# Performance work log

Hardware: AMD Instinct MI355X
Metric: run time of the kernel (lower is better)

The kernel has to match this reference:

```python
import jax, jax.numpy as jnp
import numpy as np

N_NODES = 50000
N_EDGES = 600000
IN_DIM = 128
FEAT = 128
N_CLS = 40


def _lin_params(key, fan_in, fan_out, bias=True):
    k1, k2 = jax.random.split(key)
    lim = 1.0 / np.sqrt(fan_in)
    W = jax.random.uniform(k1, (fan_out, fan_in), jnp.float32, -lim, lim)
    b = jax.random.uniform(k2, (fan_out,), jnp.float32, -lim, lim) if bias else None
    return W, b


def setup_inputs() -> dict:
    key = jax.random.key(0)
    ks = jax.random.split(key, 8)
    x = jax.random.normal(ks[0], (N_NODES, IN_DIM), jnp.float32)
    edge_index = jax.random.randint(ks[1], (2, N_EDGES), 0, N_NODES, jnp.int64 if jax.config.read('jax_enable_x64') else jnp.int32)
    Wl1, bl1 = _lin_params(ks[2], IN_DIM, FEAT)
    Wr1, _ = _lin_params(ks[3], IN_DIM, FEAT, bias=False)
    Wl2, bl2 = _lin_params(ks[4], FEAT, FEAT)
    Wr2, _ = _lin_params(ks[5], FEAT, FEAT, bias=False)
    Wl3, bl3 = _lin_params(ks[6], FEAT, FEAT)
    Wr3, _ = _lin_params(ks[7], FEAT, FEAT, bias=False)
    kc = jax.random.fold_in(key, 99)
    Wc, bc = _lin_params(kc, FEAT, N_CLS)
    return {"x": x, "edge_index": edge_index,
            "Wl1": Wl1, "bl1": bl1, "Wr1": Wr1,
            "Wl2": Wl2, "bl2": bl2, "Wr2": Wr2,
            "Wl3": Wl3, "bl3": bl3, "Wr3": Wr3,
            "Wc": Wc, "bc": bc}


def _sage_relu(x, src, dst, deg_inv, Wl, bl, Wr):
    # mean aggregation over incoming neighbors: gather at src, scatter-add at dst
    agg = jax.ops.segment_sum(x[src], dst, num_segments=N_NODES)  # [N, F]
    agg = agg * deg_inv[:, None]
    out = agg @ Wl.T + bl + x @ Wr.T  # W1*mean(neigh) + W2*x_root
    return jax.nn.relu(out)


def reference(x, edge_index, Wl1, bl1, Wr1, Wl2, bl2, Wr2, Wl3, bl3, Wr3, Wc, bc):
    src, dst = edge_index[0], edge_index[1]
    deg = jax.ops.segment_sum(jnp.ones((src.shape[0],), x.dtype), dst, num_segments=N_NODES)
    deg_inv = 1.0 / jnp.maximum(deg, 1.0)
    local_repr = _sage_relu(x, src, dst, deg_inv, Wl1, bl1, Wr1)
    global_repr = _sage_relu(local_repr, src, dst, deg_inv, Wl2, bl2, Wr2)
    # invariant_feature_extractor: one SAGEConvwithRelu + (eval-mode) dropout + residual
    h = _sage_relu(global_repr, src, dst, deg_inv, Wl3, bl3, Wr3)
    vanilla_if = h + global_repr
    vanilla_pred = vanilla_if @ Wc.T + bc
    return vanilla_pred
```

## Files before the change

### kernel.cpp

```cpp
#include <hip/hip_runtime.h>
#include <hip/hip_bf16.h>

constexpr int N_NODES = 50000;
constexpr int N_EDGES = 600000;
constexpr int D       = 128;
constexpr int N_CLS   = 40;

using bf16x8 = __attribute__((ext_vector_type(8))) short;
using f32x4  = __attribute__((ext_vector_type(4))) float;

__device__ inline unsigned short f2bf(float f) {
    __hip_bfloat16 h = __float2bfloat16(f);
    return __builtin_bit_cast(unsigned short, h);
}
__device__ inline float bf2f(unsigned short u) {
    __hip_bfloat16 h = __builtin_bit_cast(__hip_bfloat16, u);
    return __bfloat162float(h);
}


__global__ void hist_kernel(const int* __restrict__ ei, int* __restrict__ cnt) {
    int e = blockIdx.x * 256 + threadIdx.x;
    if (e < N_EDGES) atomicAdd(&cnt[ei[N_EDGES + e]], 1);
}

__global__ __launch_bounds__(1024) void scan_block_kernel(const int* __restrict__ cnt,
                                                          int* __restrict__ rs,
                                                          int* __restrict__ bsum, int n) {
    __shared__ int t[1024];
    int tid = threadIdx.x;
    int gid = blockIdx.x * 1024 + tid;
    int v = (gid < n) ? cnt[gid] : 0;
    t[tid] = v;
    __syncthreads();
    for (int off = 1; off < 1024; off <<= 1) {
        int u = (tid >= off) ? t[tid - off] : 0;
        __syncthreads();
        t[tid] += u;
        __syncthreads();
    }
    if (gid < n) rs[gid] = t[tid] - v;
    if (tid == 1023) bsum[blockIdx.x] = t[1023];
}

__global__ void scan_sums_kernel(const int* __restrict__ bsum, int* __restrict__ boff, int nblk) {
    __shared__ int t[64];
    int tid = threadIdx.x;
    int v = (tid < nblk) ? bsum[tid] : 0;
    t[tid] = v;
    __syncthreads();
    for (int off = 1; off < 64; off <<= 1) {
        int u = (tid >= off) ? t[tid - off] : 0;
        __syncthreads();
        t[tid] += u;
        __syncthreads();
    }
    if (tid < nblk) boff[tid] = t[tid] - v;
}

__global__ void finalize_kernel(const int* __restrict__ cnt, int* __restrict__ rs,
                                int* __restrict__ cursor, float* __restrict__ dinv,
                                const int* __restrict__ boff) {
    int i = blockIdx.x * 256 + threadIdx.x;
    if (i < N_NODES) {
        int v = rs[i] + boff[i >> 10];
        rs[i] = v;
        cursor[i] = v;
        dinv[i] = 1.0f / fmaxf((float)cnt[i], 1.0f);
        if (i == 0) rs[N_NODES] = N_EDGES;
    }
}

__global__ void scatter_kernel(const int* __restrict__ ei, int* __restrict__ cursor,
                               int* __restrict__ csr) {
    int e = blockIdx.x * 256 + threadIdx.x;
    if (e < N_EDGES) {
        int d = ei[N_EDGES + e];
        int p = atomicAdd(&cursor[d], 1);
        csr[p] = ei[e];
    }
}

__global__ void split_w_kernel(const float* __restrict__ Wl, const float* __restrict__ Wr,
                               unsigned short* __restrict__ hi, unsigned short* __restrict__ lo) {
    int idx = blockIdx.x * 256 + threadIdx.x;
    int n = idx >> 8, k = idx & 255;
    float v = (k < 128) ? Wl[n * 128 + k] : Wr[n * 128 + (k - 128)];
    unsigned short h = f2bf(v);
    hi[idx] = h;
    lo[idx] = f2bf(v - bf2f(h));
}

__global__ __launch_bounds__(256) void agg_kernel(const float* __restrict__ feat,
                                                  const int* __restrict__ rs,
                                                  const int* __restrict__ csr,
                                                  const float* __restrict__ dinv,
                                                  float* __restrict__ aggn) {
    int wave = threadIdx.x >> 6;
    int lane = threadIdx.x & 63;
    int node = blockIdx.x * 4 + wave;
    if (node >= N_NODES) return;
    int e0 = rs[node], e1 = rs[node + 1];
    float ax = 0.f, ay = 0.f;
    int e = e0;
    for (; e + 4 <= e1; e += 4) {
        int s0 = csr[e], s1 = csr[e + 1], s2 = csr[e + 2], s3 = csr[e + 3];
        float2 v0 = *(const float2*)&feat[(size_t)s0 * D + lane * 2];
        float2 v1 = *(const float2*)&feat[(size_t)s1 * D + lane * 2];
        float2 v2 = *(const float2*)&feat[(size_t)s2 * D + lane * 2];
        float2 v3 = *(const float2*)&feat[(size_t)s3 * D + lane * 2];
        ax += v0.x + v1.x + v2.x + v3.x;
        ay += v0.y + v1.y + v2.y + v3.y;
    }
    for (; e < e1; ++e) {
        int s = csr[e];
        float2 v = *(const float2*)&feat[(size_t)s * D + lane * 2];
        ax += v.x; ay += v.y;
    }
    float di = dinv[node];
    float2 o; o.x = ax * di; o.y = ay * di;
    *(float2*)&aggn[(size_t)node * D + lane * 2] = o;
}

__global__ __launch_bounds__(256) void gemm_mfma_kernel(const float* __restrict__ Aagg,
                                                        const float* __restrict__ Ax,
                                                        const unsigned short* __restrict__ Whi,
                                                        const unsigned short* __restrict__ Wlo,
                                                        const float* __restrict__ bias,
                                                        const float* __restrict__ resid,
                                                        float* __restrict__ outp, int M) {
    __shared__ __align__(16) unsigned short AhS[64 * 64];
    __shared__ __align__(16) unsigned short AlS[64 * 64];
    __shared__ __align__(16) unsigned short WhS[128 * 64];
    __shared__ __align__(16) unsigned short WlS[128 * 64];
    char* AhB = (char*)AhS;
    char* AlB = (char*)AlS;
    char* WhB = (char*)WhS;
    char* WlB = (char*)WlS;

    int tid = threadIdx.x;
    int lane = tid & 63;
    int wid = tid >> 6;
    int wr = wid >> 1;
    int wc = wid & 1;
    int lr = lane & 15;
    int kg = (lane >> 4) * 8;
    int row0 = blockIdx.x * 64;

    f32x4 acc[2][4];
#pragma unroll
    for (int f = 0; f < 2; ++f)
#pragma unroll
        for (int j = 0; j < 4; ++j) acc[f][j] = (f32x4){0.f, 0.f, 0.f, 0.f};

    for (int kt = 0; kt < 4; ++kt) {
        const float* Asrc = (kt < 2) ? Aagg : Ax;
        int kcol = (kt & 1) * 64;

#pragma unroll
        for (int it = 0; it < 2; ++it) {
            int slot = tid + it * 256;
            int row = slot >> 3;
            int k8 = (slot & 7) * 8;
            int gr = row0 + row;
            if (gr >= M) gr = M - 1;
            const float* p = &Asrc[(size_t)gr * D + kcol + k8];
            float4 v0 = *(const float4*)p;
            float4 v1 = *(const float4*)(p + 4);
            float fv[8] = {v0.x, v0.y, v0.z, v0.w, v1.x, v1.y, v1.z, v1.w};
            union { unsigned short u[8]; uint4 q; } ph, pl;
#pragma unroll
            for (int j = 0; j < 8; ++j) {
                unsigned short h = f2bf(fv[j]);
                ph.u[j] = h;
                pl.u[j] = f2bf(fv[j] - bf2f(h));
            }
            int boff = (row << 7) + (k8 << 1);
            boff ^= (row & 7) << 4;
            *(uint4*)(AhB + boff) = ph.q;
            *(uint4*)(AlB + boff) = pl.q;
        }
#pragma unroll
        for (int it = 0; it < 4; ++it) {
            int slot = tid + it * 256;
            int n = slot >> 3;
            int k8 = (slot & 7) * 8;
            size_t gsrc = (size_t)n * 256 + kt * 64 + k8;
            uint4 h = *(const uint4*)&Whi[gsrc];
            uint4 l = *(const uint4*)&Wlo[gsrc];
            int boff = (n << 7) + (k8 << 1);
            boff ^= (n & 7) << 4;
            *(uint4*)(WhB + boff) = h;
            *(uint4*)(WlB + boff) = l;
        }
        __syncthreads();

#pragma unroll
        for (int ks = 0; ks < 2; ++ks) {
            int kk = ks * 32 + kg;
            bf16x8 ah[2], al[2];
#pragma unroll
            for (int f = 0; f < 2; ++f) {
                int row = wr * 32 + f * 16 + lr;
                int boff = (row << 7) + (kk << 1);
                boff ^= (row & 7) << 4;
                ah[f] = *(const bf16x8*)(AhB + boff);
                al[f] = *(const bf16x8*)(AlB + boff);
            }
            bf16x8 bh[4], bl[4];
#pragma unroll
            for (int j = 0; j < 4; ++j) {
                int n = wc * 64 + j * 16 + lr;
                int boff = (n << 7) + (kk << 1);
                boff ^= (n & 7) << 4;
                bh[j] = *(const bf16x8*)(WhB + boff);
                bl[j] = *(const bf16x8*)(WlB + boff);
            }
#pragma unroll
            for (int f = 0; f < 2; ++f)
#pragma unroll
                for (int j = 0; j < 4; ++j) {
                    acc[f][j] = __builtin_amdgcn_mfma_f32_16x16x32_bf16(ah[f], bh[j], acc[f][j], 0, 0, 0);
                    acc[f][j] = __builtin_amdgcn_mfma_f32_16x16x32_bf16(ah[f], bl[j], acc[f][j], 0, 0, 0);
                    acc[f][j] = __builtin_amdgcn_mfma_f32_16x16x32_bf16(al[f], bh[j], acc[f][j], 0, 0, 0);
                }
        }
        __syncthreads();
    }

#pragma unroll
    for (int f = 0; f < 2; ++f)
#pragma unroll
        for (int j = 0; j < 4; ++j) {
            int c = wc * 64 + j * 16 + lr;
            float b = bias[c];
#pragma unroll
            for (int r = 0; r < 4; ++r) {
                int gr = row0 + wr * 32 + f * 16 + (lane >> 4) * 4 + r;
                if (gr < M) {
                    float v = acc[f][j][r] + b;
                    v = fmaxf(v, 0.f);
                    if (resid) v += resid[(size_t)gr * D + c];
                    outp[(size_t)gr * D + c] = v;
                }
            }
        }
}

__global__ __launch_bounds__(256) void classifier_kernel(const float* __restrict__ vif,
                                                         const float* __restrict__ Wc,
                                                         const float* __restrict__ bc,
                                                         float* __restrict__ outp, int M) {
    __shared__ float Vs[64][D + 4];
    __shared__ float Cs[N_CLS][D + 4];
    int tid = threadIdx.x;
    int row0 = blockIdx.x * 64;

#pragma unroll
    for (int l = 0; l < 8; ++l) {
        int slot = tid + l * 256;
        int r = slot >> 5;
        int kq = slot & 31;
        int gr = row0 + r;
        if (gr >= M) gr = M - 1;
        float4 v = *(const float4*)&vif[(size_t)gr * D + kq * 4];
        *(float4*)&Vs[r][kq * 4] = v;
    }
#pragma unroll
    for (int l = 0; l < 5; ++l) {
        int slot = tid + l * 256;
        int r = slot >> 5;
        int kq = slot & 31;
        float4 v = *(const float4*)&Wc[r * D + kq * 4];
        *(float4*)&Cs[r][kq * 4] = v;
    }
    __syncthreads();

    int r2 = tid >> 3;
    int cg = tid & 7;
    float acc[2][5] = {};
#pragma unroll 4
    for (int k4 = 0; k4 < 32; ++k4) {
        float4 a0 = *(const float4*)&Vs[r2 * 2][k4 * 4];
        float4 a1 = *(const float4*)&Vs[r2 * 2 + 1][k4 * 4];
#pragma unroll
        for (int j = 0; j < 5; ++j) {
            float4 w = *(const float4*)&Cs[cg * 5 + j][k4 * 4];
            acc[0][j] = fmaf(a0.x, w.x, fmaf(a0.y, w.y, fmaf(a0.z, w.z, fmaf(a0.w, w.w, acc[0][j]))));
            acc[1][j] = fmaf(a1.x, w.x, fmaf(a1.y, w.y, fmaf(a1.z, w.z, fmaf(a1.w, w.w, acc[1][j]))));
        }
    }
#pragma unroll
    for (int i = 0; i < 2; ++i) {
        int r = row0 + r2 * 2 + i;
        if (r >= M) continue;
#pragma unroll
        for (int j = 0; j < 5; ++j) {
            int c = cg * 5 + j;
            outp[(size_t)r * N_CLS + c] = acc[i][j] + bc[c];
        }
    }
}

extern "C" void kernel_launch(void* const* d_in, const int* in_sizes, int n_in,
                              void* d_out, int out_size, void* d_ws, size_t ws_size,
                              hipStream_t stream) {
    const float* x   = (const float*)d_in[0];
    const int*   ei  = (const int*)d_in[1];
    const float* Wl1 = (const float*)d_in[2];
    const float* bl1 = (const float*)d_in[3];
    const float* Wr1 = (const float*)d_in[4];
    const float* Wl2 = (const float*)d_in[5];
    const float* bl2 = (const float*)d_in[6];
    const float* Wr2 = (const float*)d_in[7];
    const float* Wl3 = (const float*)d_in[8];
    const float* bl3 = (const float*)d_in[9];
    const float* Wr3 = (const float*)d_in[10];
    const float* Wc  = (const float*)d_in[11];
    const float* bc  = (const float*)d_in[12];
    float* out = (float*)d_out;

    char* w = (char*)d_ws;
    size_t off = 0;
    auto carve = [&](size_t bytes) -> void* {
        void* p = w + off;
        off = (off + bytes + 255) & ~(size_t)255;
        return p;
    };
    int*   cnt    = (int*)carve((size_t)N_NODES * 4);
    int*   rs     = (int*)carve((size_t)(N_NODES + 1) * 4);
    int*   cursor = (int*)carve((size_t)N_NODES * 4);
    float* dinv   = (float*)carve((size_t)N_NODES * 4);
    int*   bsum   = (int*)carve(64 * 4);
    int*   boff   = (int*)carve(64 * 4);
    int*   csr    = (int*)carve((size_t)N_EDGES * 4);
    float* aggn   = (float*)carve((size_t)N_NODES * D * 4);
    float* bufA   = (float*)carve((size_t)N_NODES * D * 4);
    float* bufB   = (float*)carve((size_t)N_NODES * D * 4);
    unsigned short* w1h = (unsigned short*)carve(128 * 256 * 2);
    unsigned short* w1l = (unsigned short*)carve(128 * 256 * 2);
    unsigned short* w2h = (unsigned short*)carve(128 * 256 * 2);
    unsigned short* w2l = (unsigned short*)carve(128 * 256 * 2);
    unsigned short* w3h = (unsigned short*)carve(128 * 256 * 2);
    unsigned short* w3l = (unsigned short*)carve(128 * 256 * 2);
    (void)ws_size;

    const int NBLK_SCAN = (N_NODES + 1023) / 1024;
    const int GRID_E = (N_EDGES + 255) / 256;
    const int GRID_N = (N_NODES + 255) / 256;
    const int GRID_AGG = (N_NODES + 3) / 4;
    const int GRID_GEMM = (N_NODES + 63) / 64;

    hipMemsetAsync(cnt, 0, (size_t)N_NODES * 4, stream);
    hipLaunchKernelGGL(hist_kernel, dim3(GRID_E), dim3(256), 0, stream, ei, cnt);
    hipLaunchKernelGGL(split_w_kernel, dim3(128), dim3(256), 0, stream, Wl1, Wr1, w1h, w1l);
    hipLaunchKernelGGL(split_w_kernel, dim3(128), dim3(256), 0, stream, Wl2, Wr2, w2h, w2l);
    hipLaunchKernelGGL(split_w_kernel, dim3(128), dim3(256), 0, stream, Wl3, Wr3, w3h, w3l);
    hipLaunchKernelGGL(scan_block_kernel, dim3(NBLK_SCAN), dim3(1024), 0, stream, cnt, rs, bsum, N_NODES);
    hipLaunchKernelGGL(scan_sums_kernel, dim3(1), dim3(64), 0, stream, bsum, boff, NBLK_SCAN);
    hipLaunchKernelGGL(finalize_kernel, dim3(GRID_N), dim3(256), 0, stream, cnt, rs, cursor, dinv, boff);
    hipLaunchKernelGGL(scatter_kernel, dim3(GRID_E), dim3(256), 0, stream, ei, cursor, csr);

    hipLaunchKernelGGL(agg_kernel, dim3(GRID_AGG), dim3(256), 0, stream, x, rs, csr, dinv, aggn);
    hipLaunchKernelGGL(gemm_mfma_kernel, dim3(GRID_GEMM), dim3(256), 0, stream,
                       aggn, x, w1h, w1l, bl1, (const float*)nullptr, bufA, N_NODES);
    hipLaunchKernelGGL(agg_kernel, dim3(GRID_AGG), dim3(256), 0, stream, bufA, rs, csr, dinv, aggn);
    hipLaunchKernelGGL(gemm_mfma_kernel, dim3(GRID_GEMM), dim3(256), 0, stream,
                       aggn, bufA, w2h, w2l, bl2, (const float*)nullptr, bufB, N_NODES);
    hipLaunchKernelGGL(agg_kernel, dim3(GRID_AGG), dim3(256), 0, stream, bufB, rs, csr, dinv, aggn);
    hipLaunchKernelGGL(gemm_mfma_kernel, dim3(GRID_GEMM), dim3(256), 0, stream,
                       aggn, bufB, w3h, w3l, bl3, bufB, bufA, N_NODES);
    hipLaunchKernelGGL(classifier_kernel, dim3(GRID_GEMM), dim3(256), 0, stream,
                       bufA, Wc, bc, out, N_NODES);
}
```

Baseline: 391.0 us.

## Fuse neighbor aggregation into SAGE GEMM and fold classifier into last layer

Mean aggregation now runs inside the MFMA GEMM kernel: each block gathers neighbor rows via CSR into shared memory as split bf16 hi/lo tiles. This removes the aggn intermediate and its global write and read. The third layer also applies the residual and runs the classifier with MFMA in the same kernel, so bufA and the separate classifier launch are gone. Weight splitting is batched into fewer launches. In exchange, per-block gather work is serialized (16 nodes per wave), which may reduce memory-level parallelism compared with the separate agg kernel, and shared memory rises to 64KB per block, which limits occupancy.

```diff
diff --git a/kernel.cpp b/kernel.cpp
--- a/kernel.cpp
+++ b/kernel.cpp
@@ -81,62 +81,168 @@
     }
 }
 
-__global__ void split_w_kernel(const float* __restrict__ Wl, const float* __restrict__ Wr,
-                               unsigned short* __restrict__ hi, unsigned short* __restrict__ lo) {
+__global__ void split_w3_kernel(const float* __restrict__ Wl1, const float* __restrict__ Wr1,
+                                const float* __restrict__ Wl2, const float* __restrict__ Wr2,
+                                const float* __restrict__ Wl3, const float* __restrict__ Wr3,
+                                unsigned short* __restrict__ hi, unsigned short* __restrict__ lo) {
+    int layer = blockIdx.x >> 7;
+    int idx = (blockIdx.x & 127) * 256 + threadIdx.x;
+    int n = idx >> 8, k = idx & 255;
+    const float* Wl = (layer == 0) ? Wl1 : (layer == 1) ? Wl2 : Wl3;
+    const float* Wr = (layer == 0) ? Wr1 : (layer == 1) ? Wr2 : Wr3;
+    float v = (k < 128) ? Wl[n * 128 + k] : Wr[n * 128 + (k - 128)];
+    unsigned short h = f2bf(v);
+    size_t o = (size_t)layer * 32768 + idx;
+    hi[o] = h;
+    lo[o] = f2bf(v - bf2f(h));
+}
+
+__global__ void split_wc_kernel(const float* __restrict__ Wc,
+                                unsigned short* __restrict__ hi, unsigned short* __restrict__ lo) {
     int idx = blockIdx.x * 256 + threadIdx.x;
-    int n = idx >> 8, k = idx & 255;
-    float v = (k < 128) ? Wl[n * 128 + k] : Wr[n * 128 + (k - 128)];
+    int n = idx >> 7, k = idx & 127;
+    float v = (n < N_CLS) ? Wc[n * 128 + k] : 0.f;
     unsigned short h = f2bf(v);
     hi[idx] = h;
     lo[idx] = f2bf(v - bf2f(h));
 }
 
-__global__ __launch_bounds__(256) void agg_kernel(const float* __restrict__ feat,
-                                                  const int* __restrict__ rs,
-                                                  const int* __restrict__ csr,
-                                                  const float* __restrict__ dinv,
-                                                  float* __restrict__ aggn) {
-    int wave = threadIdx.x >> 6;
-    int lane = threadIdx.x & 63;
-    int node = blockIdx.x * 4 + wave;
-    if (node >= N_NODES) return;
-    int e0 = rs[node], e1 = rs[node + 1];
-    float ax = 0.f, ay = 0.f;
-    int e = e0;
-    for (; e + 4 <= e1; e += 4) {
-        int s0 = csr[e], s1 = csr[e + 1], s2 = csr[e + 2], s3 = csr[e + 3];
-        float2 v0 = *(const float2*)&feat[(size_t)s0 * D + lane * 2];
-        float2 v1 = *(const float2*)&feat[(size_t)s1 * D + lane * 2];
-        float2 v2 = *(const float2*)&feat[(size_t)s2 * D + lane * 2];
-        float2 v3 = *(const float2*)&feat[(size_t)s3 * D + lane * 2];
-        ax += v0.x + v1.x + v2.x + v3.x;
-        ay += v0.y + v1.y + v2.y + v3.y;
-    }
-    for (; e < e1; ++e) {
-        int s = csr[e];
-        float2 v = *(const float2*)&feat[(size_t)s * D + lane * 2];
-        ax += v.x; ay += v.y;
-    }
-    float di = dinv[node];
-    float2 o; o.x = ax * di; o.y = ay * di;
-    *(float2*)&aggn[(size_t)node * D + lane * 2] = o;
-}
-
-__global__ __launch_bounds__(256) void gemm_mfma_kernel(const float* __restrict__ Aagg,
-                                                        const float* __restrict__ Ax,
-                                                        const unsigned short* __restrict__ Whi,
-                                                        const unsigned short* __restrict__ Wlo,
-                                                        const float* __restrict__ bias,
-                                                        const float* __restrict__ resid,
-                                                        float* __restrict__ outp, int M) {
-    __shared__ __align__(16) unsigned short AhS[64 * 64];
-    __shared__ __align__(16) unsigned short AlS[64 * 64];
-    __shared__ __align__(16) unsigned short WhS[128 * 64];
-    __shared__ __align__(16) unsigned short WlS[128 * 64];
-    char* AhB = (char*)AhS;
-    char* AlB = (char*)AlS;
-    char* WhB = (char*)WhS;
-    char* WlB = (char*)WlS;
+
+#define GATHER_PHASE                                                             \
+    for (int i = 0; i < 16; ++i) {                                               \
+        int rloc = wid * 16 + i;                                                 \
+        int gn = row0 + rloc;                                                    \
+        if (gn >= M) gn = M - 1;                                                 \
+        int e0 = rs[gn], e1 = rs[gn + 1];                                        \
+        float ax = 0.f, ay = 0.f;                                                \
+        for (int b = e0; b < e1; b += 64) {                                      \
+            int cnt = min(64, e1 - b);                                           \
+            int idxv = (lane < cnt) ? csr[b + lane] : 0;                         \
+            int j = 0;                                                           \
+            for (; j + 8 <= cnt; j += 8) {                                       \
+                int s0 = __shfl(idxv, j + 0), s1 = __shfl(idxv, j + 1);          \
+                int s2 = __shfl(idxv, j + 2), s3 = __shfl(idxv, j + 3);          \
+                int s4 = __shfl(idxv, j + 4), s5 = __shfl(idxv, j + 5);          \
+                int s6 = __shfl(idxv, j + 6), s7 = __shfl(idxv, j + 7);          \
+                float2 v0 = *(const float2*)&feat[(size_t)s0 * D + lane * 2];    \
+                float2 v1 = *(const float2*)&feat[(size_t)s1 * D + lane * 2];    \
+                float2 v2 = *(const float2*)&feat[(size_t)s2 * D + lane * 2];    \
+                float2 v3 = *(const float2*)&feat[(size_t)s3 * D + lane * 2];    \
+                float2 v4 = *(const float2*)&feat[(size_t)s4 * D + lane * 2];    \
+                float2 v5 = *(const float2*)&feat[(size_t)s5 * D + lane * 2];    \
+                float2 v6 = *(const float2*)&feat[(size_t)s6 * D + lane * 2];    \
+                float2 v7 = *(const float2*)&feat[(size_t)s7 * D + lane * 2];    \
+                ax += v0.x + v1.x + v2.x + v3.x + v4.x + v5.x + v6.x + v7.x;     \
+                ay += v0.y + v1.y + v2.y + v3.y + v4.y + v5.y + v6.y + v7.y;     \
+            }                                                                    \
+            for (; j < cnt; ++j) {                                               \
+                int s = __shfl(idxv, j);                                         \
+                float2 v = *(const float2*)&feat[(size_t)s * D + lane * 2];      \
+                ax += v.x; ay += v.y;                                            \
+            }                                                                    \
+        }                                                                        \
+        float di = dinv[gn];                                                     \
+        ax *= di; ay *= di;                                                      \
+        unsigned short h0 = f2bf(ax), l0 = f2bf(ax - bf2f(h0));                  \
+        unsigned short h1 = f2bf(ay), l1 = f2bf(ay - bf2f(h1));                  \
+        int t = lane >> 5;                                                       \
+        int kloc = (lane * 2) & 63;                                              \
+        int boff = (rloc << 7) + (kloc << 1);                                    \
+        boff ^= (rloc & 7) << 4;                                                 \
+        *(unsigned int*)(AhT + t * 8192 + boff) = (unsigned)h0 | ((unsigned)h1 << 16); \
+        *(unsigned int*)(AlT + t * 8192 + boff) = (unsigned)l0 | ((unsigned)l1 << 16); \
+    }                                                                            \
+    __syncthreads();
+
+#define KT_LOOP                                                                  \
+    for (int kt = 0; kt < 4; ++kt) {                                             \
+        int tb = (kt < 2 ? kt : kt - 2) * 8192;                                  \
+        if (kt >= 2) {                                                           \
+            int kcol = (kt & 1) * 64;                                            \
+            _Pragma("unroll")                                                    \
+            for (int it = 0; it < 2; ++it) {                                     \
+                int slot = tid + it * 256;                                       \
+                int row = slot >> 3;                                             \
+                int k8 = (slot & 7) * 8;                                         \
+                int gr = row0 + row;                                             \
+                if (gr >= M) gr = M - 1;                                         \
+                const float* p = &feat[(size_t)gr * D + kcol + k8];              \
+                float4 v0 = *(const float4*)p;                                   \
+                float4 v1 = *(const float4*)(p + 4);                             \
+                float fv[8] = {v0.x, v0.y, v0.z, v0.w, v1.x, v1.y, v1.z, v1.w};  \
+                union { unsigned short u[8]; uint4 q; } ph, pl;                  \
+                _Pragma("unroll")                                                \
+                for (int j = 0; j < 8; ++j) {                                    \
+                    unsigned short h = f2bf(fv[j]);                              \
+                    ph.u[j] = h;                                                 \
+                    pl.u[j] = f2bf(fv[j] - bf2f(h));                             \
+                }                                                                \
+                int boff = (row << 7) + (k8 << 1);                               \
+                boff ^= (row & 7) << 4;                                          \
+                *(uint4*)(AhT + tb + boff) = ph.q;                               \
+                *(uint4*)(AlT + tb + boff) = pl.q;                               \
+            }                                                                    \
+        }                                                                        \
+        _Pragma("unroll")                                                        \
+        for (int it = 0; it < 4; ++it) {                                         \
+            int slot = tid + it * 256;                                           \
+            int n = slot >> 3;                                                   \
+            int k8 = (slot & 7) * 8;                                             \
+            size_t gsrc = (size_t)n * 256 + kt * 64 + k8;                        \
+            uint4 h = *(const uint4*)&Whi[gsrc];                                 \
+            uint4 l = *(const uint4*)&Wlo[gsrc];                                 \
+            int boff = (n << 7) + (k8 << 1);                                     \
+            boff ^= (n & 7) << 4;                                                \
+            *(uint4*)(WhB + boff) = h;                                           \
+            *(uint4*)(WlB + boff) = l;                                           \
+        }                                                                        \
+        __syncthreads();                                                         \
+        _Pragma("unroll")                                                        \
+        for (int ks = 0; ks < 2; ++ks) {                                         \
+            int kk = ks * 32 + kg;                                               \
+            bf16x8 ah[2], al[2];                                                 \
+            _Pragma("unroll")                                                    \
+            for (int f = 0; f < 2; ++f) {                                        \
+                int row = wr * 32 + f * 16 + lr;                                 \
+                int boff = (row << 7) + (kk << 1);                               \
+                boff ^= (row & 7) << 4;                                          \
+                ah[f] = *(const bf16x8*)(AhT + tb + boff);                       \
+                al[f] = *(const bf16x8*)(AlT + tb + boff);                       \
+            }                                                                    \
+            bf16x8 bh[4], bl[4];                                                 \
+            _Pragma("unroll")                                                    \
+            for (int j = 0; j < 4; ++j) {                                        \
+                int n = wc * 64 + j * 16 + lr;                                   \
+                int boff = (n << 7) + (kk << 1);                                 \
+                boff ^= (n & 7) << 4;                                            \
+                bh[j] = *(const bf16x8*)(WhB + boff);                            \
+                bl[j] = *(const bf16x8*)(WlB + boff);                            \
+            }                                                                    \
+            _Pragma("unroll")                                                    \
+            for (int f = 0; f < 2; ++f)                                          \
+                _Pragma("unroll")                                                \
+                for (int j = 0; j < 4; ++j) {                                    \
+                    acc[f][j] = __builtin_amdgcn_mfma_f32_16x16x32_bf16(ah[f], bh[j], acc[f][j], 0, 0, 0); \
+                    acc[f][j] = __builtin_amdgcn_mfma_f32_16x16x32_bf16(ah[f], bl[j], acc[f][j], 0, 0, 0); \
+                    acc[f][j] = __builtin_amdgcn_mfma_f32_16x16x32_bf16(al[f], bh[j], acc[f][j], 0, 0, 0); \
+                }                                                                \
+        }                                                                        \
+        __syncthreads();                                                         \
+    }
+
+__global__ __launch_bounds__(256) void fused_sage_kernel(const float* __restrict__ feat,
+                                                         const int* __restrict__ rs,
+                                                         const int* __restrict__ csr,
+                                                         const float* __restrict__ dinv,
+                                                         const unsigned short* __restrict__ Whi,
+                                                         const unsigned short* __restrict__ Wlo,
+                                                         const float* __restrict__ bias,
+                                                         float* __restrict__ outp, int M) {
+    __shared__ __align__(16) char smem[65536];
+    char* AhT = smem;
+    char* AlT = smem + 16384;
+    char* WhB = smem + 32768;
+    char* WlB = smem + 49152;
 
     int tid = threadIdx.x;
     int lane = tid & 63;
@@ -153,80 +259,8 @@
 #pragma unroll
         for (int j = 0; j < 4; ++j) acc[f][j] = (f32x4){0.f, 0.f, 0.f, 0.f};
 
-    for (int kt = 0; kt < 4; ++kt) {
-        const float* Asrc = (kt < 2) ? Aagg : Ax;
-        int kcol = (kt & 1) * 64;
-
-#pragma unroll
-        for (int it = 0; it < 2; ++it) {
-            int slot = tid + it * 256;
-            int row = slot >> 3;
-            int k8 = (slot & 7) * 8;
-            int gr = row0 + row;
-            if (gr >= M) gr = M - 1;
-            const float* p = &Asrc[(size_t)gr * D + kcol + k8];
-            float4 v0 = *(const float4*)p;
-            float4 v1 = *(const float4*)(p + 4);
-            float fv[8] = {v0.x, v0.y, v0.z, v0.w, v1.x, v1.y, v1.z, v1.w};
-            union { unsigned short u[8]; uint4 q; } ph, pl;
-#pragma unroll
-            for (int j = 0; j < 8; ++j) {
-                unsigned short h = f2bf(fv[j]);
-                ph.u[j] = h;
-                pl.u[j] = f2bf(fv[j] - bf2f(h));
-            }
-            int boff = (row << 7) + (k8 << 1);
-            boff ^= (row & 7) << 4;
-            *(uint4*)(AhB + boff) = ph.q;
-            *(uint4*)(AlB + boff) = pl.q;
-        }
-#pragma unroll
-        for (int it = 0; it < 4; ++it) {
-            int slot = tid + it * 256;
-            int n = slot >> 3;
-            int k8 = (slot & 7) * 8;
-            size_t gsrc = (size_t)n * 256 + kt * 64 + k8;
-            uint4 h = *(const uint4*)&Whi[gsrc];
-            uint4 l = *(const uint4*)&Wlo[gsrc];
-            int boff = (n << 7) + (k8 << 1);
-            boff ^= (n & 7) << 4;
-            *(uint4*)(WhB + boff) = h;
-            *(uint4*)(WlB + boff) = l;
-        }
-        __syncthreads();
-
-#pragma unroll
-        for (int ks = 0; ks < 2; ++ks) {
-            int kk = ks * 32 + kg;
-            bf16x8 ah[2], al[2];
-#pragma unroll
-            for (int f = 0; f < 2; ++f) {
-                int row = wr * 32 + f * 16 + lr;
-                int boff = (row << 7) + (kk << 1);
-                boff ^= (row & 7) << 4;
-                ah[f] = *(const bf16x8*)(AhB + boff);
-                al[f] = *(const bf16x8*)(AlB + boff);
-            }
-            bf16x8 bh[4], bl[4];
-#pragma unroll
-            for (int j = 0; j < 4; ++j) {
-                int n = wc * 64 + j * 16 + lr;
-                int boff = (n << 7) + (kk << 1);
-                boff ^= (n & 7) << 4;
-                bh[j] = *(const bf16x8*)(WhB + boff);
-                bl[j] = *(const bf16x8*)(WlB + boff);
-            }
-#pragma unroll
-            for (int f = 0; f < 2; ++f)
-#pragma unroll
-                for (int j = 0; j < 4; ++j) {
-                    acc[f][j] = __builtin_amdgcn_mfma_f32_16x16x32_bf16(ah[f], bh[j], acc[f][j], 0, 0, 0);
-                    acc[f][j] = __builtin_amdgcn_mfma_f32_16x16x32_bf16(ah[f], bl[j], acc[f][j], 0, 0, 0);
-                    acc[f][j] = __builtin_amdgcn_mfma_f32_16x16x32_bf16(al[f], bh[j], acc[f][j], 0, 0, 0);
-                }
-        }
-        __syncthreads();
-    }
+    GATHER_PHASE
+    KT_LOOP
 
 #pragma unroll
     for (int f = 0; f < 2; ++f)
@@ -237,67 +271,125 @@
 #pragma unroll
             for (int r = 0; r < 4; ++r) {
                 int gr = row0 + wr * 32 + f * 16 + (lane >> 4) * 4 + r;
-                if (gr < M) {
-                    float v = acc[f][j][r] + b;
-                    v = fmaxf(v, 0.f);
-                    if (resid) v += resid[(size_t)gr * D + c];
-                    outp[(size_t)gr * D + c] = v;
-                }
+                if (gr < M) outp[(size_t)gr * D + c] = fmaxf(acc[f][j][r] + b, 0.f);
             }
         }
 }
 
-__global__ __launch_bounds__(256) void classifier_kernel(const float* __restrict__ vif,
-                                                         const float* __restrict__ Wc,
-                                                         const float* __restrict__ bc,
-                                                         float* __restrict__ outp, int M) {
-    __shared__ float Vs[64][D + 4];
-    __shared__ float Cs[N_CLS][D + 4];
+__global__ __launch_bounds__(256) void fused_cls_kernel(const float* __restrict__ feat,
+                                                        const int* __restrict__ rs,
+                                                        const int* __restrict__ csr,
+                                                        const float* __restrict__ dinv,
+                                                        const unsigned short* __restrict__ Whi,
+                                                        const unsigned short* __restrict__ Wlo,
+                                                        const float* __restrict__ bias,
+                                                        const float* __restrict__ residf,
+                                                        const unsigned short* __restrict__ Wch,
+                                                        const unsigned short* __restrict__ Wcl,
+                                                        const float* __restrict__ bc,
+                                                        float* __restrict__ outp, int M) {
+    __shared__ __align__(16) char smem[65536];
+    char* AhT = smem;
+    char* AlT = smem + 16384;
+    char* WhB = smem + 32768;
+    char* WlB = smem + 49152;
+
     int tid = threadIdx.x;
+    int lane = tid & 63;
+    int wid = tid >> 6;
+    int wr = wid >> 1;
+    int wc = wid & 1;
+    int lr = lane & 15;
+    int kg = (lane >> 4) * 8;
     int row0 = blockIdx.x * 64;
 
-#pragma unroll
-    for (int l = 0; l < 8; ++l) {
-        int slot = tid + l * 256;
-        int r = slot >> 5;
-        int kq = slot & 31;
-        int gr = row0 + r;
-        if (gr >= M) gr = M - 1;
-        float4 v = *(const float4*)&vif[(size_t)gr * D + kq * 4];
-        *(float4*)&Vs[r][kq * 4] = v;
-    }
-#pragma unroll
-    for (int l = 0; l < 5; ++l) {
-        int slot = tid + l * 256;
-        int r = slot >> 5;
-        int kq = slot & 31;
-        float4 v = *(const float4*)&Wc[r * D + kq * 4];
-        *(float4*)&Cs[r][kq * 4] = v;
-    }
-    __syncthreads();
-
-    int r2 = tid >> 3;
-    int cg = tid & 7;
-    float acc[2][5] = {};
-#pragma unroll 4
-    for (int k4 = 0; k4 < 32; ++k4) {
-        float4 a0 = *(const float4*)&Vs[r2 * 2][k4 * 4];
-        float4 a1 = *(const float4*)&Vs[r2 * 2 + 1][k4 * 4];
-#pragma unroll
-        for (int j = 0; j < 5; ++j) {
-            float4 w = *(const float4*)&Cs[cg * 5 + j][k4 * 4];
-            acc[0][j] = fmaf(a0.x, w.x, fmaf(a0.y, w.y, fmaf(a0.z, w.z, fmaf(a0.w, w.w, acc[0][j]))));
-            acc[1][j] = fmaf(a1.x, w.x, fmaf(a1.y, w.y, fmaf(a1.z, w.z, fmaf(a1.w, w.w, acc[1][j]))));
+    f32x4 acc[2][4];
+#pragma unroll
+    for (int f = 0; f < 2; ++f)
+#pragma unroll
+        for (int j = 0; j < 4; ++j) acc[f][j] = (f32x4){0.f, 0.f, 0.f, 0.f};
+
+    GATHER_PHASE
+    KT_LOOP
+
+    f32x4 acc2[3];
+#pragma unroll
+    for (int j = 0; j < 3; ++j) acc2[j] = (f32x4){0.f, 0.f, 0.f, 0.f};
+
+    for (int p = 0; p < 2; ++p) {
+#pragma unroll
+        for (int it = 0; it < 2; ++it) {
+            int slot = tid + it * 256;
+            if (slot < 384) {
+                int n = slot >> 3;
+                int k8 = (slot & 7) * 8;
+                size_t gsrc = (size_t)n * 128 + p * 64 + k8;
+                uint4 h = *(const uint4*)&Wch[gsrc];
+                uint4 l = *(const uint4*)&Wcl[gsrc];
+                int boff = (n << 7) + (k8 << 1);
+                boff ^= (n & 7) << 4;
+                *(uint4*)(WhB + boff) = h;
+                *(uint4*)(WlB + boff) = l;
+            }
         }
-    }
-#pragma unroll
-    for (int i = 0; i < 2; ++i) {
-        int r = row0 + r2 * 2 + i;
-        if (r >= M) continue;
-#pragma unroll
-        for (int j = 0; j < 5; ++j) {
-            int c = cg * 5 + j;
-            outp[(size_t)r * N_CLS + c] = acc[i][j] + bc[c];
+        if (wc == p) {
+#pragma unroll
+            for (int f = 0; f < 2; ++f)
+#pragma unroll
+                for (int j = 0; j < 4; ++j) {
+                    int c = wc * 64 + j * 16 + lr;
+                    float b = bias[c];
+#pragma unroll
+                    for (int r = 0; r < 4; ++r) {
+                        int row = wr * 32 + f * 16 + (lane >> 4) * 4 + r;
+                        int gr = row0 + row;
+                        int gra = (gr < M) ? gr : (M - 1);
+                        float v = fmaxf(acc[f][j][r] + b, 0.f);
+                        v += residf[(size_t)gra * D + c];
+                        int kloc = j * 16 + lr;
+                        int boff = (row << 7) + (kloc << 1);
+                        boff ^= (row & 7) << 4;
+                        unsigned short h = f2bf(v);
+                        *(unsigned short*)(AhT + boff) = h;
+                        *(unsigned short*)(AlT + boff) = f2bf(v - bf2f(h));
+                    }
+                }
+        }
+        __syncthreads();
+
+#pragma unroll
+        for (int ks = 0; ks < 2; ++ks) {
+            int kk = ks * 32 + kg;
+            int row = wid * 16 + lr;
+            int boffA = (row << 7) + (kk << 1);
+            boffA ^= (row & 7) << 4;
+            bf16x8 ah = *(const bf16x8*)(AhT + boffA);
+            bf16x8 al = *(const bf16x8*)(AlT + boffA);
+#pragma unroll
+            for (int j = 0; j < 3; ++j) {
+                int n = j * 16 + lr;
+                int boffB = (n << 7) + (kk << 1);
+                boffB ^= (n & 7) << 4;
+                bf16x8 bh = *(const bf16x8*)(WhB + boffB);
+                bf16x8 bl = *(const bf16x8*)(WlB + boffB);
+                acc2[j] = __builtin_amdgcn_mfma_f32_16x16x32_bf16(ah, bh, acc2[j], 0, 0, 0);
+                acc2[j] = __builtin_amdgcn_mfma_f32_16x16x32_bf16(ah, bl, acc2[j], 0, 0, 0);
+                acc2[j] = __builtin_amdgcn_mfma_f32_16x16x32_bf16(al, bh, acc2[j], 0, 0, 0);
+            }
+        }
+        __syncthreads();
+    }
+
+#pragma unroll
+    for (int j = 0; j < 3; ++j) {
+        int c = j * 16 + lr;
+        if (c < N_CLS) {
+            float b = bc[c];
+#pragma unroll
+            for (int r = 0; r < 4; ++r) {
+                int gr = row0 + wid * 16 + (lane >> 4) * 4 + r;
+                if (gr < M) outp[(size_t)gr * N_CLS + c] = acc2[j][r] + b;
+            }
         }
     }
 }
@@ -334,42 +426,34 @@
     int*   bsum   = (int*)carve(64 * 4);
     int*   boff   = (int*)carve(64 * 4);
     int*   csr    = (int*)carve((size_t)N_EDGES * 4);
-    float* aggn   = (float*)carve((size_t)N_NODES * D * 4);
     float* bufA   = (float*)carve((size_t)N_NODES * D * 4);
     float* bufB   = (float*)carve((size_t)N_NODES * D * 4);
-    unsigned short* w1h = (unsigned short*)carve(128 * 256 * 2);
-    unsigned short* w1l = (unsigned short*)carve(128 * 256 * 2);
-    unsigned short* w2h = (unsigned short*)carve(128 * 256 * 2);
-    unsigned short* w2l = (unsigned short*)carve(128 * 256 * 2);
-    unsigned short* w3h = (unsigned short*)carve(128 * 256 * 2);
-    unsigned short* w3l = (unsigned short*)carve(128 * 256 * 2);
+    unsigned short* w123h = (unsigned short*)carve(3 * 128 * 256 * 2);
+    unsigned short* w123l = (unsigned short*)carve(3 * 128 * 256 * 2);
+    unsigned short* wch   = (unsigned short*)carve(48 * 128 * 2);
+    unsigned short* wcl   = (unsigned short*)carve(48 * 128 * 2);
     (void)ws_size;
 
     const int NBLK_SCAN = (N_NODES + 1023) / 1024;
     const int GRID_E = (N_EDGES + 255) / 256;
     const int GRID_N = (N_NODES + 255) / 256;
-    const int GRID_AGG = (N_NODES + 3) / 4;
     const int GRID_GEMM = (N_NODES + 63) / 64;
 
     hipMemsetAsync(cnt, 0, (size_t)N_NODES * 4, stream);
     hipLaunchKernelGGL(hist_kernel, dim3(GRID_E), dim3(256), 0, stream, ei, cnt);
-    hipLaunchKernelGGL(split_w_kernel, dim3(128), dim3(256), 0, stream, Wl1, Wr1, w1h, w1l);
-    hipLaunchKernelGGL(split_w_kernel, dim3(128), dim3(256), 0, stream, Wl2, Wr2, w2h, w2l);
-    hipLaunchKernelGGL(split_w_kernel, dim3(128), dim3(256), 0, stream, Wl3, Wr3, w3h, w3l);
+    hipLaunchKernelGGL(split_w3_kernel, dim3(384), dim3(256), 0, stream,
+                       Wl1, Wr1, Wl2, Wr2, Wl3, Wr3, w123h, w123l);
+    hipLaunchKernelGGL(split_wc_kernel, dim3(24), dim3(256), 0, stream, Wc, wch, wcl);
     hipLaunchKernelGGL(scan_block_kernel, dim3(NBLK_SCAN), dim3(1024), 0, stream, cnt, rs, bsum, N_NODES);
     hipLaunchKernelGGL(scan_sums_kernel, dim3(1), dim3(64), 0, stream, bsum, boff, NBLK_SCAN);
     hipLaunchKernelGGL(finalize_kernel, dim3(GRID_N), dim3(256), 0, stream, cnt, rs, cursor, dinv, boff);
     hipLaunchKernelGGL(scatter_kernel, dim3(GRID_E), dim3(256), 0, stream, ei, cursor, csr);
 
-    hipLaunchKernelGGL(agg_kernel, dim3(GRID_AGG), dim3(256), 0, stream, x, rs, csr, dinv, aggn);
-    hipLaunchKernelGGL(gemm_mfma_kernel, dim3(GRID_GEMM), dim3(256), 0, stream,
-                       aggn, x, w1h, w1l, bl1, (const float*)nullptr, bufA, N_NODES);
-    hipLaunchKernelGGL(agg_kernel, dim3(GRID_AGG), dim3(256), 0, stream, bufA, rs, csr, dinv, aggn);
-    hipLaunchKernelGGL(gemm_mfma_kernel, dim3(GRID_GEMM), dim3(256), 0, stream,
-                       aggn, bufA, w2h, w2l, bl2, (const float*)nullptr, bufB, N_NODES);
-    hipLaunchKernelGGL(agg_kernel, dim3(GRID_AGG), dim3(256), 0, stream, bufB, rs, csr, dinv, aggn);
-    hipLaunchKernelGGL(gemm_mfma_kernel, dim3(GRID_GEMM), dim3(256), 0, stream,
-                       aggn, bufB, w3h, w3l, bl3, bufB, bufA, N_NODES);
-    hipLaunchKernelGGL(classifier_kernel, dim3(GRID_GEMM), dim3(256), 0, stream,
-                       bufA, Wc, bc, out, N_NODES);
-}
+    hipLaunchKernelGGL(fused_sage_kernel, dim3(GRID_GEMM), dim3(256), 0, stream,
+                       x, rs, csr, dinv, w123h, w123l, bl1, bufA, N_NODES);
+    hipLaunchKernelGGL(fused_sage_kernel, dim3(GRID_GEMM), dim3(256), 0, stream,
+                       bufA, rs, csr, dinv, w123h + 32768, w123l + 32768, bl2, bufB, N_NODES);
+    hipLaunchKernelGGL(fused_cls_kernel, dim3(GRID_GEMM), dim3(256), 0, stream,
+                       bufB, rs, csr, dinv, w123h + 65536, w123l + 65536, bl3, bufB,
+                       wch, wcl, bc, out, N_NODES);
+}
```

Result: slower. 494.3 us (+26.4%).
